# Kernel optimization log

Measured on AMD Instinct MI355X. Metric: run time of the kernel, lower is better.

The kernel has to match this reference:

```python
import jax, jax.numpy as jnp
import numpy as np

B, N, L, H, N_NODE, STEP = 512, 50, 50, 128, 100000, 1


def setup_inputs() -> dict:
    key = jax.random.key(0)
    ks = jax.random.split(key, 24)
    stdv = 1.0 / np.sqrt(H)
    u = lambda k, shape: jax.random.uniform(k, shape, jnp.float32, -stdv, stdv)
    inp = {
        "items": jax.random.randint(ks[0], (B, N), 0, N_NODE),
        "A": jax.random.uniform(ks[1], (B, N, 2 * N), jnp.float32),
        "alias_inputs": jax.random.randint(ks[2], (B, L), 0, N),
        "embedding": u(ks[3], (N_NODE, H)),
        "w_ih": u(ks[4], (3 * H, 2 * H)),
        "w_hh": u(ks[5], (3 * H, H)),
        "b_ih": u(ks[6], (3 * H,)),
        "b_hh": u(ks[7], (3 * H,)),
        "b_iah": u(ks[8], (H,)),
        "b_oah": u(ks[9], (H,)),
        "W_ein": u(ks[10], (H, H)), "b_ein": u(ks[11], (H,)),
        "W_eout": u(ks[12], (H, H)), "b_eout": u(ks[13], (H,)),
        "W1": u(ks[14], (H, H)), "b1": u(ks[15], (H,)),
        "W2": u(ks[16], (H, H)), "b2": u(ks[17], (H,)),
        "W3": u(ks[18], (1, H)),
        "Wt": u(ks[19], (H, 2 * H)), "bt": u(ks[20], (H,)),
    }
    return inp


def reference(items, A, alias_inputs, embedding, w_ih, w_hh, b_ih, b_hh,
              b_iah, b_oah, W_ein, b_ein, W_eout, b_eout,
              W1, b1, W2, b2, W3, Wt, bt):
    hidden = embedding[items]  # [B,N,H]
    A_in, A_out = A[:, :, :N], A[:, :, N:2 * N]
    for _ in range(STEP):
        # GRU-style GNN cell
        h_in = jnp.matmul(A_in, hidden @ W_ein.T + b_ein) + b_iah   # [B,N,H]
        h_out = jnp.matmul(A_out, hidden @ W_eout.T + b_eout) + b_oah
        inputs = jnp.concatenate([h_in, h_out], axis=2)             # [B,N,2H]
        gi = inputs @ w_ih.T + b_ih                                  # [B,N,3H]
        gh = hidden @ w_hh.T + b_hh
        i_r, i_i, i_n = jnp.split(gi, 3, axis=2)
        h_r, h_i, h_n = jnp.split(gh, 3, axis=2)
        resetgate = jax.nn.sigmoid(i_r + h_r)
        inputgate = jax.nn.sigmoid(i_i + h_i)
        newgate = jnp.tanh(i_n + resetgate * h_n)
        hidden = newgate + inputgate * (hidden - newgate)
    # gather per-position node states: seq_hidden[b, l] = hidden[b, alias[b, l]]
    mask = alias_inputs > 0  # [B,L]
    idx = jnp.broadcast_to(alias_inputs[:, :, None], (B, L, H))
    seq_hidden = jnp.take_along_axis(hidden, idx, axis=1)  # [B,L,H]
    last = jnp.sum(mask, axis=1) - 1
    ht = seq_hidden[jnp.arange(B), last]  # [B,H]
    # attention pooling
    q1 = (ht @ W1.T + b1)[:, None, :]      # [B,1,H]
    q2 = seq_hidden @ W2.T + b2            # [B,L,H]
    alpha = jax.nn.sigmoid(q1 + q2) @ W3.T  # [B,L,1]
    a = jnp.sum(alpha * seq_hidden * mask[:, :, None].astype(seq_hidden.dtype), axis=1)
    a = jnp.concatenate([a, ht], axis=1) @ Wt.T + bt  # [B,H]
    scores = a @ embedding[1:].T  # [B, n_node-1]
    return scores
```

## Files before the change

kernel.cpp:

```cpp
#include <hip/hip_runtime.h>

#define NB   512
#define NN   50
#define LLn  50
#define HD   128
#define OUTN 99999

#define WS_W1T   0
#define WS_W2T   65536
#define WS_WTT   131072
#define WS_WEH   262144
#define WS_WEL   327680
#define WS_WCATH 393216
#define WS_WCATL 688128
#define WS_AHI   983040
#define WS_ALO   1114112
#define WS_W2H   1245184
#define WS_W2L   1277952


typedef __attribute__((ext_vector_type(8))) short bf16x8;
typedef __attribute__((ext_vector_type(4))) float f32x4;

__device__ __forceinline__ unsigned short f2bf(float f) {
  unsigned int u = __float_as_uint(f);
  unsigned int r = (u + 0x7FFFu + ((u >> 16) & 1u)) >> 16;
  return (unsigned short)r;
}
__device__ __forceinline__ float bf2f(unsigned short h) {
  return __uint_as_float(((unsigned int)h) << 16);
}
__device__ __forceinline__ void cvt4(float4 v, ushort4& hi, ushort4& lo) {
  unsigned short h0 = f2bf(v.x), h1 = f2bf(v.y), h2 = f2bf(v.z), h3 = f2bf(v.w);
  hi = make_ushort4(h0, h1, h2, h3);
  lo = make_ushort4(f2bf(v.x - bf2f(h0)), f2bf(v.y - bf2f(h1)),
                    f2bf(v.z - bf2f(h2)), f2bf(v.w - bf2f(h3)));
}
__device__ __forceinline__ void gl_lds16(const void* g, void* l) {
  __builtin_amdgcn_global_load_lds(
      (const __attribute__((address_space(1))) void*)g,
      (__attribute__((address_space(3))) void*)l, 16, 0, 0);
}
__device__ __forceinline__ float sigm(float x) { return 1.f/(1.f + __expf(-x)); }

__global__ void k0_prep(const float* __restrict__ w_ih, const float* __restrict__ w_hh,
                        const float* __restrict__ W_ein, const float* __restrict__ W_eout,
                        const float* __restrict__ W1, const float* __restrict__ W2,
                        const float* __restrict__ Wt, char* __restrict__ wsb)
{
  float* wsf = (float*)wsb;
  for (int i = blockIdx.x * blockDim.x + threadIdx.x; i < 262144; i += gridDim.x * blockDim.x) {
    int idx = i;
    if (idx < 16384) { int k = idx >> 7, c = idx & 127; wsf[idx] = W1[c*128 + k]; continue; }
    idx -= 16384;
    if (idx < 16384) { int k = idx >> 7, c = idx & 127; wsf[16384 + idx] = W2[c*128 + k]; continue; }
    idx -= 16384;
    if (idx < 32768) { int k = idx >> 7, c = idx & 127; wsf[32768 + idx] = Wt[c*256 + k]; continue; }
    idx -= 32768;
    if (idx < 32768) {
      int n = idx >> 7, k = idx & 127;
      float v = (n < 128) ? W_ein[n*128 + k] : W_eout[(n-128)*128 + k];
      unsigned short h = f2bf(v);
      *(unsigned short*)(wsb + WS_WEH + idx*2) = h;
      *(unsigned short*)(wsb + WS_WEL + idx*2) = f2bf(v - bf2f(h));
      continue;
    }
    idx -= 32768;
    if (idx < 147456) {
      int n = idx / 384, k = idx % 384;
      float v = (k < 256) ? w_ih[n*256 + k] : w_hh[n*128 + (k - 256)];
      unsigned short h = f2bf(v);
      *(unsigned short*)(wsb + WS_WCATH + idx*2) = h;
      *(unsigned short*)(wsb + WS_WCATL + idx*2) = f2bf(v - bf2f(h));
      continue;
    }
    idx -= 147456;
    {
      float v = W2[idx];
      unsigned short h = f2bf(v);
      *(unsigned short*)(wsb + WS_W2H + idx*2) = h;
      *(unsigned short*)(wsb + WS_W2L + idx*2) = f2bf(v - bf2f(h));
    }
  }
}

__global__ __launch_bounds__(512) void k1f(const int* __restrict__ items,
    const float* __restrict__ A, const float* __restrict__ emb,
    const int* __restrict__ alias_in,
    const float* __restrict__ b_ein, const float* __restrict__ b_eout,
    const float* __restrict__ b_iah, const float* __restrict__ b_oah,
    const float* __restrict__ b_ih, const float* __restrict__ b_hh,
    const float* __restrict__ b1, const float* __restrict__ b2,
    const float* __restrict__ W3, const float* __restrict__ bt_,
    char* __restrict__ wsb)
{
  extern __shared__ char lds[];
  char*  IMG0H = lds;
  char*  IMG0L = lds + 16384;
  float* SIG   = (float*)lds;
  char*  HH    = lds + 32768;
  char*  HL    = lds + 49152;
  char*  HETH  = lds + 65536;
  char*  HETL  = lds + 98304;
  char*  IMG1H = lds + 65536;
  char*  IMG1L = lds + 81920;
  char*  H2H   = lds + 65536;
  char*  H2L   = lds + 81920;
  float* H2f   = (float*)(lds + 98304);
  float* Q1P   = (float*)(lds + 32768);
  float* AP    = (float*)(lds + 34816);
  float* RP    = (float*)(lds + 36864);
  float* ALP   = (float*)(lds + 38912);
  int*   ALI   = (int*)(lds + 39168);

  const int b = blockIdx.x, tid = threadIdx.x;
  const int lane = tid & 63, wid = tid >> 6, l15 = lane & 15, lq = lane >> 4;

  for (int i = tid; i < 7168; i += 512) {
    int bufsel = (i >= 3584), e = bufsel ? i - 3584 : i;
    int cc = e / 14, m = 50 + e % 14;
    unsigned adr = (unsigned)(cc*128) + (((unsigned)(m*2)) ^ (((unsigned)(cc&7)) << 4));
    *(unsigned short*)((bufsel ? HETL : HETH) + adr) = 0;
  }
  {
    const float* Ab = A + (size_t)b*NN*100;
    for (int i = tid; i < 8192; i += 512) {
      int sel = i >> 12, e = i & 4095, n = e >> 6, m = e & 63;
      float v = (n < 50 && m < 50) ? Ab[n*100 + sel*50 + m] : 0.f;
      unsigned short hi = f2bf(v);
      unsigned short lo = f2bf(v - bf2f(hi));
      unsigned adr = (unsigned)(n*128) + (((unsigned)(m*2)) ^ (((unsigned)(n&7)) << 4));
      *(unsigned short*)(lds + sel*16384 + adr) = hi;
      *(unsigned short*)(lds + sel*16384 + 8192 + adr) = lo;
    }
  }
  for (int i = tid; i < 2048; i += 512) {
    int row = i >> 5, part = i & 31;
    float4 v = make_float4(0.f,0.f,0.f,0.f);
    if (row < 50) {
      int it = items[b*NN + row];
      v = *(const float4*)&emb[(size_t)it*128 + part*4];
    }
    ushort4 h4v, g4v;
    cvt4(v, h4v, g4v);
    unsigned off = row*256 + (((unsigned)(part*8)) ^ (((unsigned)(row&7)) << 4));
    *(ushort4*)(HH + off) = h4v;
    *(ushort4*)(HL + off) = g4v;
  }
  __syncthreads();

  {
    f32x4 acc2[4][2];
#pragma unroll
    for (int i = 0; i < 4; ++i) { acc2[i][0] = (f32x4){0,0,0,0}; acc2[i][1] = (f32x4){0,0,0,0}; }
    for (int s = 0; s < 4; ++s) {
      bf16x8 ah[4], al[4];
#pragma unroll
      for (int i = 0; i < 4; ++i) {
        int row = i*16 + l15;
        unsigned off = row*256 + (((unsigned)(s*64 + lq*16)) ^ (((unsigned)(row&7)) << 4));
        ah[i] = *(const bf16x8*)(HH + off);
        al[i] = *(const bf16x8*)(HL + off);
      }
#pragma unroll
      for (int j = 0; j < 2; ++j) {
        int nc = wid*32 + j*16 + l15;
        unsigned boff = (unsigned)(nc*256 + s*64 + lq*16);
        bf16x8 bh = *(const bf16x8*)(wsb + WS_WEH + boff);
        bf16x8 bl = *(const bf16x8*)(wsb + WS_WEL + boff);
#pragma unroll
        for (int i = 0; i < 4; ++i) {
          acc2[i][j] = __builtin_amdgcn_mfma_f32_16x16x32_bf16(ah[i], bh, acc2[i][j], 0,0,0);
          acc2[i][j] = __builtin_amdgcn_mfma_f32_16x16x32_bf16(ah[i], bl, acc2[i][j], 0,0,0);
          acc2[i][j] = __builtin_amdgcn_mfma_f32_16x16x32_bf16(al[i], bh, acc2[i][j], 0,0,0);
        }
      }
    }
#pragma unroll
    for (int j = 0; j < 2; ++j) {
      int nc = wid*32 + j*16 + l15;
      float bv = (nc < 128) ? b_ein[nc] : b_eout[nc - 128];
#pragma unroll
      for (int i = 0; i < 4; ++i)
#pragma unroll
        for (int q = 0; q < 4; ++q) {
          int m = i*16 + lq*4 + q;
          if (m < 50) {
            float v = acc2[i][j][q] + bv;
            unsigned short hi = f2bf(v);
            unsigned short lo = f2bf(v - bf2f(hi));
            unsigned adr = (unsigned)(nc*128) + (((unsigned)(m*2)) ^ (((unsigned)(nc&7)) << 4));
            *(unsigned short*)(HETH + adr) = hi;
            *(unsigned short*)(HETL + adr) = lo;
          }
        }
    }
  }
  __syncthreads();

  {
    const int c = wid*16 + l15;
    f32x4 accS[2][4];
#pragma unroll
    for (int sel = 0; sel < 2; ++sel)
#pragma unroll
      for (int i = 0; i < 4; ++i) accS[sel][i] = (f32x4){0,0,0,0};
#pragma unroll
    for (int sel = 0; sel < 2; ++sel) {
#pragma unroll
      for (int s2 = 0; s2 < 2; ++s2) {
        int ct = sel*128 + c;
        unsigned badr = (unsigned)(ct*128) + (((unsigned)(s2*64 + lq*16)) ^ (((unsigned)(ct&7)) << 4));
        bf16x8 bh = *(const bf16x8*)(HETH + badr);
        bf16x8 bl = *(const bf16x8*)(HETL + badr);
#pragma unroll
        for (int i = 0; i < 4; ++i) {
          int n = i*16 + l15;
          unsigned aadr = (unsigned)(n*128) + (((unsigned)(s2*64 + lq*16)) ^ (((unsigned)(n&7)) << 4));
          bf16x8 ah = *(const bf16x8*)(lds + sel*16384 + aadr);
          bf16x8 al = *(const bf16x8*)(lds + sel*16384 + 8192 + aadr);
          accS[sel][i] = __builtin_amdgcn_mfma_f32_16x16x32_bf16(ah, bh, accS[sel][i], 0,0,0);
          accS[sel][i] = __builtin_amdgcn_mfma_f32_16x16x32_bf16(ah, bl, accS[sel][i], 0,0,0);
          accS[sel][i] = __builtin_amdgcn_mfma_f32_16x16x32_bf16(al, bh, accS[sel][i], 0,0,0);
        }
      }
    }
    __syncthreads();
#pragma unroll
    for (int sel = 0; sel < 2; ++sel) {
      float bv = sel ? b_oah[c] : b_iah[c];
      char* dH = sel ? IMG1H : IMG0H;
      char* dL = sel ? IMG1L : IMG0L;
#pragma unroll
      for (int i = 0; i < 4; ++i)
#pragma unroll
        for (int q = 0; q < 4; ++q) {
          int row = i*16 + lq*4 + q;
          float v = accS[sel][i][q] + bv;
          unsigned short hi = f2bf(v);
          unsigned short lo = f2bf(v - bf2f(hi));
          unsigned adr = row*256 + (((unsigned)(c*2)) ^ (((unsigned)(row&7)) << 4));
          *(unsigned short*)(dH + adr) = hi;
          *(unsigned short*)(dL + adr) = lo;
        }
    }
  }
  __syncthreads();

  f32x4 accRI[4][2], accNi[4], accNh[4];
#pragma unroll
  for (int i = 0; i < 4; ++i) {
    accRI[i][0] = (f32x4){0,0,0,0}; accRI[i][1] = (f32x4){0,0,0,0};
    accNi[i] = (f32x4){0,0,0,0};    accNh[i] = (f32x4){0,0,0,0};
  }
  const int nl = wid*16 + l15;

  auto cat_gemm = [&](const char* AH, const char* AL, int kh, bool toNh) {
    for (int s = 0; s < 4; ++s) {
      bf16x8 ah[4], al[4];
#pragma unroll
      for (int i = 0; i < 4; ++i) {
        int row = i*16 + l15;
        unsigned off = row*256 + (((unsigned)(s*64 + lq*16)) ^ (((unsigned)(row&7)) << 4));
        ah[i] = *(const bf16x8*)(AH + off);
        al[i] = *(const bf16x8*)(AL + off);
      }
#pragma unroll
      for (int g = 0; g < 2; ++g) {
        unsigned boff = (unsigned)((g*128 + nl)*768 + kh*256 + s*64 + lq*16);
        bf16x8 bh = *(const bf16x8*)(wsb + WS_WCATH + boff);
        bf16x8 bl = *(const bf16x8*)(wsb + WS_WCATL + boff);
#pragma unroll
        for (int i = 0; i < 4; ++i) {
          accRI[i][g] = __builtin_amdgcn_mfma_f32_16x16x32_bf16(ah[i], bh, accRI[i][g], 0,0,0);
          accRI[i][g] = __builtin_amdgcn_mfma_f32_16x16x32_bf16(ah[i], bl, accRI[i][g], 0,0,0);
          accRI[i][g] = __builtin_amdgcn_mfma_f32_16x16x32_bf16(al[i], bh, accRI[i][g], 0,0,0);
        }
      }
      {
        unsigned boff = (unsigned)((256 + nl)*768 + kh*256 + s*64 + lq*16);
        bf16x8 bh = *(const bf16x8*)(wsb + WS_WCATH + boff);
        bf16x8 bl = *(const bf16x8*)(wsb + WS_WCATL + boff);
        if (toNh) {
#pragma unroll
          for (int i = 0; i < 4; ++i) {
            accNh[i] = __builtin_amdgcn_mfma_f32_16x16x32_bf16(ah[i], bh, accNh[i], 0,0,0);
            accNh[i] = __builtin_amdgcn_mfma_f32_16x16x32_bf16(ah[i], bl, accNh[i], 0,0,0);
            accNh[i] = __builtin_amdgcn_mfma_f32_16x16x32_bf16(al[i], bh, accNh[i], 0,0,0);
          }
        } else {
#pragma unroll
          for (int i = 0; i < 4; ++i) {
            accNi[i] = __builtin_amdgcn_mfma_f32_16x16x32_bf16(ah[i], bh, accNi[i], 0,0,0);
            accNi[i] = __builtin_amdgcn_mfma_f32_16x16x32_bf16(ah[i], bl, accNi[i], 0,0,0);
            accNi[i] = __builtin_amdgcn_mfma_f32_16x16x32_bf16(al[i], bh, accNi[i], 0,0,0);
          }
        }
      }
    }
  };

  cat_gemm(IMG0H, IMG0L, 0, false);
  cat_gemm(IMG1H, IMG1L, 1, false);
  cat_gemm(HH,    HL,    2, true);
  __syncthreads();

  {
    const int c = nl;
    float bir = b_ih[c], bii = b_ih[128+c], bin_ = b_ih[256+c];
    float bhr = b_hh[c], bhi = b_hh[128+c], bhn  = b_hh[256+c];
#pragma unroll
    for (int i = 0; i < 4; ++i) {
#pragma unroll
      for (int q = 0; q < 4; ++q) {
        int row = i*16 + lq*4 + q;
        if (row < 50) {
          float rg = sigm(accRI[i][0][q] + bir + bhr);
          float ig = sigm(accRI[i][1][q] + bii + bhi);
          float ng_ = tanhf(accNi[i][q] + bin_ + rg*(accNh[i][q] + bhn));
          unsigned byte = row*256 + (((unsigned)(c*2)) ^ (((unsigned)(row&7)) << 4));
          float h = bf2f(*(const unsigned short*)(HH + byte))
                  + bf2f(*(const unsigned short*)(HL + byte));
          float hn = ng_ + ig*(h - ng_);
          H2f[row*128 + c] = hn;
          unsigned short hi = f2bf(hn);
          unsigned short lo = f2bf(hn - bf2f(hi));
          *(unsigned short*)(H2H + byte) = hi;
          *(unsigned short*)(H2L + byte) = lo;
        }
      }
    }
  }
  __syncthreads();

  if (tid < 64) ALI[tid] = (tid < LLn) ? alias_in[b*LLn + tid] : 0;
  __syncthreads();

  int cnt = 0;
  for (int l = 0; l < LLn; ++l) cnt += (ALI[l] > 0) ? 1 : 0;
  int last = cnt - 1; if (last < 0) last = LLn - 1;
  const int a_last = ALI[last];

  const int c = tid & 127, h4 = tid >> 7;
  const float* W1T = (const float*)(wsb + WS_W1T);
  const float* WtT = (const float*)(wsb + WS_WTT);

  {
    float q = 0.f;
    for (int k = h4*32; k < h4*32 + 32; k += 4) {
      float4 x = *(const float4*)&H2f[a_last*128 + k];
      q += x.x*W1T[(k<<7)+c] + x.y*W1T[((k+1)<<7)+c]
         + x.z*W1T[((k+2)<<7)+c] + x.w*W1T[((k+3)<<7)+c];
    }
    Q1P[h4*128 + c] = q;
  }
  __syncthreads();

  {
    const int cq = nl;
    f32x4 qa[4];
#pragma unroll
    for (int i = 0; i < 4; ++i) qa[i] = (f32x4){0,0,0,0};
    for (int s = 0; s < 4; ++s) {
      unsigned boff = (unsigned)(cq*256 + s*64 + lq*16);
      bf16x8 bh = *(const bf16x8*)(wsb + WS_W2H + boff);
      bf16x8 bl = *(const bf16x8*)(wsb + WS_W2L + boff);
#pragma unroll
      for (int i = 0; i < 4; ++i) {
        int ali = ALI[i*16 + l15];
        unsigned aadr = ali*256 + (((unsigned)(s*64 + lq*16)) ^ (((unsigned)(ali&7)) << 4));
        bf16x8 ah = *(const bf16x8*)(H2H + aadr);
        bf16x8 al = *(const bf16x8*)(H2L + aadr);
        qa[i] = __builtin_amdgcn_mfma_f32_16x16x32_bf16(ah, bh, qa[i], 0,0,0);
        qa[i] = __builtin_amdgcn_mfma_f32_16x16x32_bf16(ah, bl, qa[i], 0,0,0);
        qa[i] = __builtin_amdgcn_mfma_f32_16x16x32_bf16(al, bh, qa[i], 0,0,0);
      }
    }
    float q1c = Q1P[cq] + Q1P[128+cq] + Q1P[256+cq] + Q1P[384+cq] + b1[cq] + b2[cq];
#pragma unroll
    for (int i = 0; i < 4; ++i)
#pragma unroll
      for (int q = 0; q < 4; ++q) {
        int l = i*16 + lq*4 + q;
        if (l < 50) SIG[l*128 + cq] = sigm(q1c + qa[i][q]);
      }
  }
  __syncthreads();

  if (tid < 400) {
    int l = tid >> 3, qd = tid & 7;
    float sum = 0.f;
    for (int cc = qd*16; cc < qd*16 + 16; cc += 4) {
      float4 x = *(const float4*)&SIG[l*128 + cc];
      sum += x.x*W3[cc] + x.y*W3[cc+1] + x.z*W3[cc+2] + x.w*W3[cc+3];
    }
    sum += __shfl_xor(sum, 1);
    sum += __shfl_xor(sum, 2);
    sum += __shfl_xor(sum, 4);
    if (qd == 0) ALP[l] = (ALI[l] > 0) ? sum : 0.f;
  }
  __syncthreads();

  {
    float acc = 0.f;
    int l0 = h4*13, l1 = l0 + 13; if (l1 > LLn) l1 = LLn;
    for (int l = l0; l < l1; ++l)
      acc += ALP[l] * H2f[ALI[l]*128 + c];
    AP[h4*128 + c] = acc;
  }
  __syncthreads();

  {
    float r = 0.f;
    for (int k = h4*32; k < h4*32 + 32; ++k) {
      float av = AP[k] + AP[128+k] + AP[256+k] + AP[384+k];
      r += av * WtT[(k<<7) + c] + H2f[a_last*128 + k] * WtT[((128+k)<<7) + c];
    }
    RP[h4*128 + c] = r;
  }
  __syncthreads();

  if (tid < 128) {
    float r = bt_[c] + RP[c] + RP[128+c] + RP[256+c] + RP[384+c];
    int kh = c >> 6, kl = c & 63;
    unsigned int cb = (unsigned int)(kl*2) ^ (((unsigned int)(b & 7)) << 4);
    unsigned short hi = f2bf(r);
    unsigned short lo = f2bf(r - bf2f(hi));
    *(unsigned short*)(wsb + WS_AHI + kh*65536 + b*128 + cb) = hi;
    *(unsigned short*)(wsb + WS_ALO + kh*65536 + b*128 + cb) = lo;
  }
}

__global__ __launch_bounds__(512) void k2_mfma(const float* __restrict__ emb,
                                               const char* __restrict__ wsb,
                                               float* __restrict__ out)
{
  extern __shared__ char ldsc[];
  char* AHI = ldsc;
  char* ALO = ldsc + 32768;
  char* EHI = ldsc + 65536;
  char* ELO = ldsc + 81920;

  const int tid  = threadIdx.x;
  const int lane = tid & 63;
  const int wid  = tid >> 6;
  const int wm   = wid >> 1;
  const int wn   = wid & 1;
  const int j0   = blockIdx.x * 128;
  const int l15  = lane & 15, lq = lane >> 4;

  f32x4 acc[2][4][4];
#pragma unroll
  for (int bi = 0; bi < 2; ++bi)
#pragma unroll
    for (int i = 0; i < 4; ++i)
#pragma unroll
      for (int j = 0; j < 4; ++j) acc[bi][i][j] = (f32x4){0.f, 0.f, 0.f, 0.f};

  for (int kh = 0; kh < 2; ++kh) {
    {
      int rbase = tid >> 4, c4 = tid & 15;
#pragma unroll
      for (int rr = 0; rr < 4; ++rr) {
        int row = rbase + rr*32;
        int j = j0 + row; if (j > OUTN - 1) j = OUTN - 1;
        float4 v = *(const float4*)&emb[(size_t)(1 + j)*HD + kh*64 + c4*4];
        ushort4 hi4, lo4;
        cvt4(v, hi4, lo4);
        unsigned int off = (unsigned int)(row*128) + (((unsigned int)(c4*8)) ^ (((unsigned int)(row&7)) << 4));
        *(ushort4*)(EHI + off) = hi4;
        *(ushort4*)(ELO + off) = lo4;
      }
    }
#pragma unroll
    for (int bi = 0; bi < 2; ++bi) {
      const char* srcH = wsb + WS_AHI + kh*65536 + bi*32768;
      const char* srcL = wsb + WS_ALO + kh*65536 + bi*32768;
#pragma unroll
      for (int r = 0; r < 4; ++r) {
        int off = (r*512 + tid) * 16;
        gl_lds16(srcH + off, AHI + off);
        gl_lds16(srcL + off, ALO + off);
      }
      __syncthreads();

#pragma unroll
      for (int s = 0; s < 2; ++s) {
        bf16x8 ah[4], al[4], bh[4], bl[4];
        const unsigned int cb = (unsigned int)(s*64 + (lq << 4));
#pragma unroll
        for (int i = 0; i < 4; ++i) {
          int row = wm*64 + i*16 + l15;
          unsigned int off = (unsigned int)(row*128) + (cb ^ (((unsigned int)(row&7)) << 4));
          ah[i] = *(const bf16x8*)(AHI + off);
          al[i] = *(const bf16x8*)(ALO + off);
        }
#pragma unroll
        for (int j = 0; j < 4; ++j) {
          int row = wn*64 + j*16 + l15;
          unsigned int off = (unsigned int)(row*128) + (cb ^ (((unsigned int)(row&7)) << 4));
          bh[j] = *(const bf16x8*)(EHI + off);
          bl[j] = *(const bf16x8*)(ELO + off);
        }
#pragma unroll
        for (int i = 0; i < 4; ++i)
#pragma unroll
          for (int j = 0; j < 4; ++j) {
            acc[bi][i][j] = __builtin_amdgcn_mfma_f32_16x16x32_bf16(ah[i], bh[j], acc[bi][i][j], 0, 0, 0);
            acc[bi][i][j] = __builtin_amdgcn_mfma_f32_16x16x32_bf16(ah[i], bl[j], acc[bi][i][j], 0, 0, 0);
            acc[bi][i][j] = __builtin_amdgcn_mfma_f32_16x16x32_bf16(al[i], bh[j], acc[bi][i][j], 0, 0, 0);
          }
      }
      __syncthreads();
    }
  }

#pragma unroll
  for (int bi = 0; bi < 2; ++bi)
#pragma unroll
    for (int i = 0; i < 4; ++i) {
#pragma unroll
      for (int j = 0; j < 4; ++j) {
        int jj = j0 + wn*64 + j*16 + l15;
        if (jj < OUTN) {
          size_t rowbase = (size_t)(bi*256 + wm*64 + i*16 + lq*4);
#pragma unroll
          for (int q = 0; q < 4; ++q)
            out[(rowbase + q)*OUTN + jj] = acc[bi][i][j][q];
        }
      }
    }
}

extern "C" void kernel_launch(void* const* d_in, const int* in_sizes, int n_in,
                              void* d_out, int out_size, void* d_ws, size_t ws_size,
                              hipStream_t stream)
{
  const int*   items  = (const int*)  d_in[0];
  const float* A      = (const float*)d_in[1];
  const int*   alias  = (const int*)  d_in[2];
  const float* emb    = (const float*)d_in[3];
  const float* w_ih   = (const float*)d_in[4];
  const float* w_hh   = (const float*)d_in[5];
  const float* b_ih   = (const float*)d_in[6];
  const float* b_hh   = (const float*)d_in[7];
  const float* b_iah  = (const float*)d_in[8];
  const float* b_oah  = (const float*)d_in[9];
  const float* W_ein  = (const float*)d_in[10];
  const float* b_ein  = (const float*)d_in[11];
  const float* W_eout = (const float*)d_in[12];
  const float* b_eout = (const float*)d_in[13];
  const float* W1     = (const float*)d_in[14];
  const float* b1     = (const float*)d_in[15];
  const float* W2     = (const float*)d_in[16];
  const float* b2     = (const float*)d_in[17];
  const float* W3     = (const float*)d_in[18];
  const float* Wt     = (const float*)d_in[19];
  const float* bt_    = (const float*)d_in[20];

  char*  wsb  = (char*)d_ws;
  float* outf = (float*)d_out;

  k0_prep<<<240, 256, 0, stream>>>(w_ih, w_hh, W_ein, W_eout, W1, W2, Wt, wsb);

  k1f<<<NB, 512, 131072, stream>>>(items, A, emb, alias, b_ein, b_eout, b_iah, b_oah,
                                   b_ih, b_hh, b1, b2, W3, bt_, wsb);

  k2_mfma<<<dim3(782, 1), 512, 98304, stream>>>(emb, (const char*)d_ws, outf);
}
```

Measured before the change: 181.4 us.

## Double k1f block to 1024 threads and redistribute per-wave GEMM tiles

Launches the per-batch GNN kernel with 1024 threads (16 waves) instead of 512, splitting each MFMA stage across twice as many waves: the edge GEMM gives one 16-column tile per wave, the adjacency GEMM assigns in/out to separate wave halves, and the GRU GEMM splits rows across two wave groups. The scalar attention/pooling reductions are split 8-way, and the partial-sum LDS buffers are enlarged and moved. This aims to cut per-block latency, since only 512 blocks with 128KB LDS each run at one block per CU. The cost is higher register pressure under the 1024-thread launch bound and more reduction partials.

```diff
diff --git a/kernel.cpp b/kernel.cpp
--- a/kernel.cpp
+++ b/kernel.cpp
@@ -84,7 +84,7 @@
   }
 }
 
-__global__ __launch_bounds__(512) void k1f(const int* __restrict__ items,
+__global__ __launch_bounds__(1024) void k1f(const int* __restrict__ items,
     const float* __restrict__ A, const float* __restrict__ emb,
     const int* __restrict__ alias_in,
     const float* __restrict__ b_ein, const float* __restrict__ b_eout,
@@ -108,15 +108,15 @@
   char*  H2L   = lds + 81920;
   float* H2f   = (float*)(lds + 98304);
   float* Q1P   = (float*)(lds + 32768);
-  float* AP    = (float*)(lds + 34816);
-  float* RP    = (float*)(lds + 36864);
-  float* ALP   = (float*)(lds + 38912);
-  int*   ALI   = (int*)(lds + 39168);
+  float* AP    = (float*)(lds + 36864);
+  float* RP    = (float*)(lds + 40960);
+  float* ALP   = (float*)(lds + 45056);
+  int*   ALI   = (int*)(lds + 45312);
 
   const int b = blockIdx.x, tid = threadIdx.x;
   const int lane = tid & 63, wid = tid >> 6, l15 = lane & 15, lq = lane >> 4;
 
-  for (int i = tid; i < 7168; i += 512) {
+  for (int i = tid; i < 7168; i += 1024) {
     int bufsel = (i >= 3584), e = bufsel ? i - 3584 : i;
     int cc = e / 14, m = 50 + e % 14;
     unsigned adr = (unsigned)(cc*128) + (((unsigned)(m*2)) ^ (((unsigned)(cc&7)) << 4));
@@ -124,7 +124,7 @@
   }
   {
     const float* Ab = A + (size_t)b*NN*100;
-    for (int i = tid; i < 8192; i += 512) {
+    for (int i = tid; i < 8192; i += 1024) {
       int sel = i >> 12, e = i & 4095, n = e >> 6, m = e & 63;
       float v = (n < 50 && m < 50) ? Ab[n*100 + sel*50 + m] : 0.f;
       unsigned short hi = f2bf(v);
@@ -134,7 +134,7 @@
       *(unsigned short*)(lds + sel*16384 + 8192 + adr) = lo;
     }
   }
-  for (int i = tid; i < 2048; i += 512) {
+  for (int i = tid; i < 2048; i += 1024) {
     int row = i >> 5, part = i & 31;
     float4 v = make_float4(0.f,0.f,0.f,0.f);
     if (row < 50) {
@@ -150,117 +150,100 @@
   __syncthreads();
 
   {
-    f32x4 acc2[4][2];
-#pragma unroll
-    for (int i = 0; i < 4; ++i) { acc2[i][0] = (f32x4){0,0,0,0}; acc2[i][1] = (f32x4){0,0,0,0}; }
+    f32x4 acc2[4];
+#pragma unroll
+    for (int i = 0; i < 4; ++i) acc2[i] = (f32x4){0,0,0,0};
+    const int nc = wid*16 + l15;
     for (int s = 0; s < 4; ++s) {
-      bf16x8 ah[4], al[4];
+      unsigned boff = (unsigned)(nc*256 + s*64 + lq*16);
+      bf16x8 bh = *(const bf16x8*)(wsb + WS_WEH + boff);
+      bf16x8 bl = *(const bf16x8*)(wsb + WS_WEL + boff);
 #pragma unroll
       for (int i = 0; i < 4; ++i) {
         int row = i*16 + l15;
         unsigned off = row*256 + (((unsigned)(s*64 + lq*16)) ^ (((unsigned)(row&7)) << 4));
-        ah[i] = *(const bf16x8*)(HH + off);
-        al[i] = *(const bf16x8*)(HL + off);
-      }
-#pragma unroll
-      for (int j = 0; j < 2; ++j) {
-        int nc = wid*32 + j*16 + l15;
-        unsigned boff = (unsigned)(nc*256 + s*64 + lq*16);
-        bf16x8 bh = *(const bf16x8*)(wsb + WS_WEH + boff);
-        bf16x8 bl = *(const bf16x8*)(wsb + WS_WEL + boff);
-#pragma unroll
-        for (int i = 0; i < 4; ++i) {
-          acc2[i][j] = __builtin_amdgcn_mfma_f32_16x16x32_bf16(ah[i], bh, acc2[i][j], 0,0,0);
-          acc2[i][j] = __builtin_amdgcn_mfma_f32_16x16x32_bf16(ah[i], bl, acc2[i][j], 0,0,0);
-          acc2[i][j] = __builtin_amdgcn_mfma_f32_16x16x32_bf16(al[i], bh, acc2[i][j], 0,0,0);
-        }
-      }
-    }
-#pragma unroll
-    for (int j = 0; j < 2; ++j) {
-      int nc = wid*32 + j*16 + l15;
-      float bv = (nc < 128) ? b_ein[nc] : b_eout[nc - 128];
-#pragma unroll
-      for (int i = 0; i < 4; ++i)
-#pragma unroll
-        for (int q = 0; q < 4; ++q) {
-          int m = i*16 + lq*4 + q;
-          if (m < 50) {
-            float v = acc2[i][j][q] + bv;
-            unsigned short hi = f2bf(v);
-            unsigned short lo = f2bf(v - bf2f(hi));
-            unsigned adr = (unsigned)(nc*128) + (((unsigned)(m*2)) ^ (((unsigned)(nc&7)) << 4));
-            *(unsigned short*)(HETH + adr) = hi;
-            *(unsigned short*)(HETL + adr) = lo;
-          }
-        }
-    }
-  }
-  __syncthreads();
-
-  {
-    const int c = wid*16 + l15;
-    f32x4 accS[2][4];
-#pragma unroll
-    for (int sel = 0; sel < 2; ++sel)
-#pragma unroll
-      for (int i = 0; i < 4; ++i) accS[sel][i] = (f32x4){0,0,0,0};
-#pragma unroll
-    for (int sel = 0; sel < 2; ++sel) {
-#pragma unroll
-      for (int s2 = 0; s2 < 2; ++s2) {
-        int ct = sel*128 + c;
-        unsigned badr = (unsigned)(ct*128) + (((unsigned)(s2*64 + lq*16)) ^ (((unsigned)(ct&7)) << 4));
-        bf16x8 bh = *(const bf16x8*)(HETH + badr);
-        bf16x8 bl = *(const bf16x8*)(HETL + badr);
-#pragma unroll
-        for (int i = 0; i < 4; ++i) {
-          int n = i*16 + l15;
-          unsigned aadr = (unsigned)(n*128) + (((unsigned)(s2*64 + lq*16)) ^ (((unsigned)(n&7)) << 4));
-          bf16x8 ah = *(const bf16x8*)(lds + sel*16384 + aadr);
-          bf16x8 al = *(const bf16x8*)(lds + sel*16384 + 8192 + aadr);
-          accS[sel][i] = __builtin_amdgcn_mfma_f32_16x16x32_bf16(ah, bh, accS[sel][i], 0,0,0);
-          accS[sel][i] = __builtin_amdgcn_mfma_f32_16x16x32_bf16(ah, bl, accS[sel][i], 0,0,0);
-          accS[sel][i] = __builtin_amdgcn_mfma_f32_16x16x32_bf16(al, bh, accS[sel][i], 0,0,0);
-        }
-      }
-    }
-    __syncthreads();
-#pragma unroll
-    for (int sel = 0; sel < 2; ++sel) {
-      float bv = sel ? b_oah[c] : b_iah[c];
-      char* dH = sel ? IMG1H : IMG0H;
-      char* dL = sel ? IMG1L : IMG0L;
-#pragma unroll
-      for (int i = 0; i < 4; ++i)
-#pragma unroll
-        for (int q = 0; q < 4; ++q) {
-          int row = i*16 + lq*4 + q;
-          float v = accS[sel][i][q] + bv;
+        bf16x8 ah = *(const bf16x8*)(HH + off);
+        bf16x8 al = *(const bf16x8*)(HL + off);
+        acc2[i] = __builtin_amdgcn_mfma_f32_16x16x32_bf16(ah, bh, acc2[i], 0,0,0);
+        acc2[i] = __builtin_amdgcn_mfma_f32_16x16x32_bf16(ah, bl, acc2[i], 0,0,0);
+        acc2[i] = __builtin_amdgcn_mfma_f32_16x16x32_bf16(al, bh, acc2[i], 0,0,0);
+      }
+    }
+    float bv = (nc < 128) ? b_ein[nc] : b_eout[nc - 128];
+#pragma unroll
+    for (int i = 0; i < 4; ++i)
+#pragma unroll
+      for (int q = 0; q < 4; ++q) {
+        int m = i*16 + lq*4 + q;
+        if (m < 50) {
+          float v = acc2[i][q] + bv;
           unsigned short hi = f2bf(v);
           unsigned short lo = f2bf(v - bf2f(hi));
-          unsigned adr = row*256 + (((unsigned)(c*2)) ^ (((unsigned)(row&7)) << 4));
-          *(unsigned short*)(dH + adr) = hi;
-          *(unsigned short*)(dL + adr) = lo;
-        }
-    }
-  }
-  __syncthreads();
-
-  f32x4 accRI[4][2], accNi[4], accNh[4];
-#pragma unroll
-  for (int i = 0; i < 4; ++i) {
+          unsigned adr = (unsigned)(nc*128) + (((unsigned)(m*2)) ^ (((unsigned)(nc&7)) << 4));
+          *(unsigned short*)(HETH + adr) = hi;
+          *(unsigned short*)(HETL + adr) = lo;
+        }
+      }
+  }
+  __syncthreads();
+
+  {
+    const int sel = wid >> 3;
+    const int c   = (wid & 7)*16 + l15;
+    f32x4 accS[4];
+#pragma unroll
+    for (int i = 0; i < 4; ++i) accS[i] = (f32x4){0,0,0,0};
+#pragma unroll
+    for (int s2 = 0; s2 < 2; ++s2) {
+      int ct = sel*128 + c;
+      unsigned badr = (unsigned)(ct*128) + (((unsigned)(s2*64 + lq*16)) ^ (((unsigned)(ct&7)) << 4));
+      bf16x8 bh = *(const bf16x8*)(HETH + badr);
+      bf16x8 bl = *(const bf16x8*)(HETL + badr);
+#pragma unroll
+      for (int i = 0; i < 4; ++i) {
+        int n = i*16 + l15;
+        unsigned aadr = (unsigned)(n*128) + (((unsigned)(s2*64 + lq*16)) ^ (((unsigned)(n&7)) << 4));
+        bf16x8 ah = *(const bf16x8*)(lds + sel*16384 + aadr);
+        bf16x8 al = *(const bf16x8*)(lds + sel*16384 + 8192 + aadr);
+        accS[i] = __builtin_amdgcn_mfma_f32_16x16x32_bf16(ah, bh, accS[i], 0,0,0);
+        accS[i] = __builtin_amdgcn_mfma_f32_16x16x32_bf16(ah, bl, accS[i], 0,0,0);
+        accS[i] = __builtin_amdgcn_mfma_f32_16x16x32_bf16(al, bh, accS[i], 0,0,0);
+      }
+    }
+    __syncthreads();
+    float bv = sel ? b_oah[c] : b_iah[c];
+    char* dH = sel ? IMG1H : IMG0H;
+    char* dL = sel ? IMG1L : IMG0L;
+#pragma unroll
+    for (int i = 0; i < 4; ++i)
+#pragma unroll
+      for (int q = 0; q < 4; ++q) {
+        int row = i*16 + lq*4 + q;
+        float v = accS[i][q] + bv;
+        unsigned short hi = f2bf(v);
+        unsigned short lo = f2bf(v - bf2f(hi));
+        unsigned adr = row*256 + (((unsigned)(c*2)) ^ (((unsigned)(row&7)) << 4));
+        *(unsigned short*)(dH + adr) = hi;
+        *(unsigned short*)(dL + adr) = lo;
+      }
+  }
+  __syncthreads();
+
+  const int wm = wid >> 3, wn = wid & 7;
+  const int nl = wn*16 + l15;
+  f32x4 accRI[2][2], accNi[2], accNh[2];
+#pragma unroll
+  for (int i = 0; i < 2; ++i) {
     accRI[i][0] = (f32x4){0,0,0,0}; accRI[i][1] = (f32x4){0,0,0,0};
     accNi[i] = (f32x4){0,0,0,0};    accNh[i] = (f32x4){0,0,0,0};
   }
-  const int nl = wid*16 + l15;
 
   auto cat_gemm = [&](const char* AH, const char* AL, int kh, bool toNh) {
     for (int s = 0; s < 4; ++s) {
-      bf16x8 ah[4], al[4];
-#pragma unroll
-      for (int i = 0; i < 4; ++i) {
-        int row = i*16 + l15;
+      bf16x8 ah[2], al[2];
+#pragma unroll
+      for (int i = 0; i < 2; ++i) {
+        int row = wm*32 + i*16 + l15;
         unsigned off = row*256 + (((unsigned)(s*64 + lq*16)) ^ (((unsigned)(row&7)) << 4));
         ah[i] = *(const bf16x8*)(AH + off);
         al[i] = *(const bf16x8*)(AL + off);
@@ -271,7 +254,7 @@
         bf16x8 bh = *(const bf16x8*)(wsb + WS_WCATH + boff);
         bf16x8 bl = *(const bf16x8*)(wsb + WS_WCATL + boff);
 #pragma unroll
-        for (int i = 0; i < 4; ++i) {
+        for (int i = 0; i < 2; ++i) {
           accRI[i][g] = __builtin_amdgcn_mfma_f32_16x16x32_bf16(ah[i], bh, accRI[i][g], 0,0,0);
           accRI[i][g] = __builtin_amdgcn_mfma_f32_16x16x32_bf16(ah[i], bl, accRI[i][g], 0,0,0);
           accRI[i][g] = __builtin_amdgcn_mfma_f32_16x16x32_bf16(al[i], bh, accRI[i][g], 0,0,0);
@@ -283,14 +266,14 @@
         bf16x8 bl = *(const bf16x8*)(wsb + WS_WCATL + boff);
         if (toNh) {
 #pragma unroll
-          for (int i = 0; i < 4; ++i) {
+          for (int i = 0; i < 2; ++i) {
             accNh[i] = __builtin_amdgcn_mfma_f32_16x16x32_bf16(ah[i], bh, accNh[i], 0,0,0);
             accNh[i] = __builtin_amdgcn_mfma_f32_16x16x32_bf16(ah[i], bl, accNh[i], 0,0,0);
             accNh[i] = __builtin_amdgcn_mfma_f32_16x16x32_bf16(al[i], bh, accNh[i], 0,0,0);
           }
         } else {
 #pragma unroll
-          for (int i = 0; i < 4; ++i) {
+          for (int i = 0; i < 2; ++i) {
             accNi[i] = __builtin_amdgcn_mfma_f32_16x16x32_bf16(ah[i], bh, accNi[i], 0,0,0);
             accNi[i] = __builtin_amdgcn_mfma_f32_16x16x32_bf16(ah[i], bl, accNi[i], 0,0,0);
             accNi[i] = __builtin_amdgcn_mfma_f32_16x16x32_bf16(al[i], bh, accNi[i], 0,0,0);
@@ -310,10 +293,10 @@
     float bir = b_ih[c], bii = b_ih[128+c], bin_ = b_ih[256+c];
     float bhr = b_hh[c], bhi = b_hh[128+c], bhn  = b_hh[256+c];
 #pragma unroll
-    for (int i = 0; i < 4; ++i) {
+    for (int i = 0; i < 2; ++i) {
 #pragma unroll
       for (int q = 0; q < 4; ++q) {
-        int row = i*16 + lq*4 + q;
+        int row = wm*32 + i*16 + lq*4 + q;
         if (row < 50) {
           float rg = sigm(accRI[i][0][q] + bir + bhr);
           float ig = sigm(accRI[i][1][q] + bii + bhi);
@@ -341,23 +324,23 @@
   int last = cnt - 1; if (last < 0) last = LLn - 1;
   const int a_last = ALI[last];
 
-  const int c = tid & 127, h4 = tid >> 7;
+  const int c = tid & 127, h8 = tid >> 7;
   const float* W1T = (const float*)(wsb + WS_W1T);
   const float* WtT = (const float*)(wsb + WS_WTT);
 
   {
     float q = 0.f;
-    for (int k = h4*32; k < h4*32 + 32; k += 4) {
+    for (int k = h8*16; k < h8*16 + 16; k += 4) {
       float4 x = *(const float4*)&H2f[a_last*128 + k];
       q += x.x*W1T[(k<<7)+c] + x.y*W1T[((k+1)<<7)+c]
          + x.z*W1T[((k+2)<<7)+c] + x.w*W1T[((k+3)<<7)+c];
     }
-    Q1P[h4*128 + c] = q;
-  }
-  __syncthreads();
-
-  {
-    const int cq = nl;
+    Q1P[h8*128 + c] = q;
+  }
+  __syncthreads();
+
+  if (wid < 8) {
+    const int cq = wid*16 + l15;
     f32x4 qa[4];
 #pragma unroll
     for (int i = 0; i < 4; ++i) qa[i] = (f32x4){0,0,0,0};
@@ -376,7 +359,9 @@
         qa[i] = __builtin_amdgcn_mfma_f32_16x16x32_bf16(al, bh, qa[i], 0,0,0);
       }
     }
-    float q1c = Q1P[cq] + Q1P[128+cq] + Q1P[256+cq] + Q1P[384+cq] + b1[cq] + b2[cq];
+    float q1c = b1[cq] + b2[cq];
+#pragma unroll
+    for (int j = 0; j < 8; ++j) q1c += Q1P[j*128 + cq];
 #pragma unroll
     for (int i = 0; i < 4; ++i)
 #pragma unroll
@@ -403,25 +388,29 @@
 
   {
     float acc = 0.f;
-    int l0 = h4*13, l1 = l0 + 13; if (l1 > LLn) l1 = LLn;
+    int l0 = h8*7, l1 = l0 + 7; if (l1 > LLn) l1 = LLn;
     for (int l = l0; l < l1; ++l)
       acc += ALP[l] * H2f[ALI[l]*128 + c];
-    AP[h4*128 + c] = acc;
+    AP[h8*128 + c] = acc;
   }
   __syncthreads();
 
   {
     float r = 0.f;
-    for (int k = h4*32; k < h4*32 + 32; ++k) {
-      float av = AP[k] + AP[128+k] + AP[256+k] + AP[384+k];
+    for (int k = h8*16; k < h8*16 + 16; ++k) {
+      float av = 0.f;
+#pragma unroll
+      for (int j = 0; j < 8; ++j) av += AP[j*128 + k];
       r += av * WtT[(k<<7) + c] + H2f[a_last*128 + k] * WtT[((128+k)<<7) + c];
     }
-    RP[h4*128 + c] = r;
+    RP[h8*128 + c] = r;
   }
   __syncthreads();
 
   if (tid < 128) {
-    float r = bt_[c] + RP[c] + RP[128+c] + RP[256+c] + RP[384+c];
+    float r = bt_[c];
+#pragma unroll
+    for (int j = 0; j < 8; ++j) r += RP[j*128 + c];
     int kh = c >> 6, kl = c & 63;
     unsigned int cb = (unsigned int)(kl*2) ^ (((unsigned int)(b & 7)) << 4);
     unsigned short hi = f2bf(r);
@@ -563,8 +552,8 @@
 
   k0_prep<<<240, 256, 0, stream>>>(w_ih, w_hh, W_ein, W_eout, W1, W2, Wt, wsb);
 
-  k1f<<<NB, 512, 131072, stream>>>(items, A, emb, alias, b_ein, b_eout, b_iah, b_oah,
-                                   b_ih, b_hh, b1, b2, W3, bt_, wsb);
+  k1f<<<NB, 1024, 131072, stream>>>(items, A, emb, alias, b_ein, b_eout, b_iah, b_oah,
+                                    b_ih, b_hh, b1, b2, W3, bt_, wsb);
 
   k2_mfma<<<dim3(782, 1), 512, 98304, stream>>>(emb, (const char*)d_ws, outf);
 }
```

New measurement: 204.6 us. 12.8% more time.
